# Optimization experiments

Hardware: AMD Instinct MI355X
Metric: run time of the kernel (lower is better)

## Reference

```python
import jax, jax.numpy as jnp
import numpy as np

T, B, IN, H1, H2, H3 = 128, 256, 512, 1024, 1024, 512


def _glorot(key, shape, fan):
    bound = 1.0 / np.sqrt(fan)
    return jax.random.uniform(key, shape, jnp.float32, -bound, bound)


def _cell_params(key, in_dim, h_dim):
    k = jax.random.split(key, 4)
    return (_glorot(k[0], (4 * h_dim, in_dim), h_dim),
            _glorot(k[1], (4 * h_dim, h_dim), h_dim),
            _glorot(k[2], (4 * h_dim,), h_dim),
            _glorot(k[3], (4 * h_dim,), h_dim))


def setup_inputs() -> dict:
    key = jax.random.key(0)
    ks = jax.random.split(key, 4)
    x = jax.random.normal(ks[0], (T, B, IN), jnp.float32)
    Wih1, Whh1, bih1, bhh1 = _cell_params(ks[1], IN, H1)
    Wih2, Whh2, bih2, bhh2 = _cell_params(ks[2], H1, H2)
    Wih3, Whh3, bih3, bhh3 = _cell_params(ks[3], H2, H3)
    return dict(input_seq=x,
                Wih1=Wih1, Whh1=Whh1, bih1=bih1, bhh1=bhh1,
                Wih2=Wih2, Whh2=Whh2, bih2=bih2, bhh2=bhh2,
                Wih3=Wih3, Whh3=Whh3, bih3=bih3, bhh3=bhh3)


def _lstm_cell(x, h, c, Wih, Whh, bih, bhh):
    # PyTorch LSTMCell gate order: i, f, g, o
    gates = x @ Wih.T + bih + h @ Whh.T + bhh
    i, f, g, o = jnp.split(gates, 4, axis=-1)
    c_new = jax.nn.sigmoid(f) * c + jax.nn.sigmoid(i) * jnp.tanh(g)
    h_new = jax.nn.sigmoid(o) * jnp.tanh(c_new)
    return h_new, c_new


def reference(input_seq, Wih1, Whh1, bih1, bhh1,
              Wih2, Whh2, bih2, bhh2,
              Wih3, Whh3, bih3, bhh3):
    Bn = input_seq.shape[1]
    init = (jnp.zeros((Bn, H1)), jnp.zeros((Bn, H1)),
            jnp.zeros((Bn, H2)), jnp.zeros((Bn, H2)),
            jnp.zeros((Bn, H3)), jnp.zeros((Bn, H3)))

    def step(carry, x_t):
        h1, c1, h2, c2, h3, c3 = carry
        h1, c1 = _lstm_cell(x_t, h1, c1, Wih1, Whh1, bih1, bhh1)
        h2, c2 = _lstm_cell(h1, h2, c2, Wih2, Whh2, bih2, bhh2)
        h3, c3 = _lstm_cell(h2, h3, c3, Wih3, Whh3, bih3, bhh3)
        return (h1, c1, h2, c2, h3, c3), None

    final, _ = jax.lax.scan(step, init, input_seq)
    return final
```

## Files before the change

### kernel.cpp

```cpp
#include <hip/hip_runtime.h>
#include <hip/hip_bf16.h>
#include <cstdint>
#include <cstddef>


typedef __attribute__((ext_vector_type(8))) short short8;
typedef __attribute__((ext_vector_type(4))) short short4v;
typedef __attribute__((ext_vector_type(4))) float floatx4;

#define NBLK 256
#define NTHR 1024

__device__ __forceinline__ float fsig(float x) {
    x = fminf(fmaxf(x, -30.f), 30.f);
    return 1.f / (1.f + __expf(-x));
}
__device__ __forceinline__ float ftanh(float x) {
    x = fminf(fmaxf(x, -15.f), 15.f);
    float e = __expf(2.f * x);
    return (e - 1.f) / (e + 1.f);
}

__device__ __forceinline__ int get_xcc() {
    int x;
    asm volatile("s_getreg_b32 %0, hwreg(HW_REG_XCC_ID)" : "=s"(x));
    return x & 7;
}


__device__ __forceinline__ void safe_sync(int* sy) {
    __syncthreads();
    if (threadIdx.x == 0) {
        int a = __hip_atomic_fetch_add(sy + 704, 1, __ATOMIC_ACQ_REL, __HIP_MEMORY_SCOPE_AGENT);
        if (a == NBLK - 1)
            __hip_atomic_store(sy + 768, 1, __ATOMIC_RELEASE, __HIP_MEMORY_SCOPE_AGENT);
        while (__hip_atomic_load(sy + 768, __ATOMIC_RELAXED, __HIP_MEMORY_SCOPE_AGENT) == 0)
            __builtin_amdgcn_s_sleep(2);
        __builtin_amdgcn_fence(__ATOMIC_ACQUIRE, "agent");
    }
    __syncthreads();
}

__device__ __forceinline__ void grid_sync(int* sy, int myx, int myM, int G) {
    __syncthreads();
    if (threadIdx.x == 0) {
        int* gen = sy + 576;
        int g = __hip_atomic_load(gen, __ATOMIC_RELAXED, __HIP_MEMORY_SCOPE_AGENT);
        int a = __hip_atomic_fetch_add(sy + myx * 64, 1, __ATOMIC_RELAXED, __HIP_MEMORY_SCOPE_AGENT);
        if ((a + 1) % myM == 0) {
            __builtin_amdgcn_fence(__ATOMIC_RELEASE, "agent");
            int m = __hip_atomic_fetch_add(sy + 512, 1, __ATOMIC_RELAXED, __HIP_MEMORY_SCOPE_AGENT);
            if ((m + 1) % G == 0)
                __hip_atomic_fetch_add(gen, 1, __ATOMIC_RELEASE, __HIP_MEMORY_SCOPE_AGENT);
        }
        while (__hip_atomic_load(gen, __ATOMIC_RELAXED, __HIP_MEMORY_SCOPE_AGENT) == g)
            __builtin_amdgcn_s_sleep(2);
        __builtin_amdgcn_fence(__ATOMIC_ACQUIRE, "agent");
    }
    __syncthreads();
}

template<int K1, int K2, int H>
__global__ void pack_frag_kernel(const float* __restrict__ Wih,
                                 const float* __restrict__ Whh,
                                 __hip_bfloat16* __restrict__ dst) {
    constexpr int NK = (K1 + K2) / 32;
    constexpr int NTT = H / 4;
    int idx = blockIdx.x * 256 + threadIdx.x;
    if (idx >= NTT * NK * 64) return;
    int slot = idx & 63;
    int kc = (idx >> 6) % NK;
    int b = idx / (64 * NK);
    int du = slot & 3, g = (slot >> 2) & 3, ksub = slot >> 4;
    int unit = b * 4 + du;
    int j = g * H + unit;
    int k0 = kc * 32 + ksub * 8;
    __hip_bfloat16 tmp[8];
#pragma unroll
    for (int e = 0; e < 8; ++e) {
        int k = k0 + e;
        float v = (k < K1) ? Wih[(size_t)j * K1 + k] : Whh[(size_t)j * K2 + (k - K1)];
        tmp[e] = __float2bfloat16(v);
    }
    *(short8*)(dst + (size_t)idx * 8) = *(short8*)tmp;
}

__global__ void pack_bias_kernel(const float* __restrict__ a,
                                 const float* __restrict__ b,
                                 int n, float* __restrict__ out) {
    int i = blockIdx.x * 256 + threadIdx.x;
    if (i < n) out[i] = a[i] + b[i];
}

__global__ void x_to_slab_kernel(const float* __restrict__ x,
                                 __hip_bfloat16* __restrict__ xs) {
    int idx = blockIdx.x * 256 + threadIdx.x;
    int j   = idx & 7;
    int row = (idx >> 3) & 255;
    int s   = (idx >> 11) & 63;
    int t   = idx >> 17;
    xs[idx] = __float2bfloat16(x[((size_t)(t * 256 + row)) * 512 + s * 8 + j]);
}

__global__ void zero_f32_kernel(float* p, int n) {
    int i = blockIdx.x * 256 + threadIdx.x;
    if (i < n) p[i] = 0.f;
}

__global__ void zero_i32_kernel(int* p, int n) {
    int i = blockIdx.x * 256 + threadIdx.x;
    if (i < n) p[i] = 0;
}

__device__ __forceinline__ short8 afrag8(const __hip_bfloat16* __restrict__ base, int k) {
    return *(const short8*)(base + (size_t)k * 8192);
}
__device__ __forceinline__ short8 afrag4(const __hip_bfloat16* __restrict__ base, int k) {
    const __hip_bfloat16* p = base + (size_t)k * 8192;
    short4v lo = *(const short4v*)p;
    short4v hi = *(const short4v*)(p + 1024);
    return (short8){lo.x, lo.y, lo.z, lo.w, hi.x, hi.y, hi.z, hi.w};
}

template<int NK1, int NK2, bool A2W4, int NT, int H, int TSTR>
__device__ __forceinline__ void run_layer(
    const short8* __restrict__ ldsw, int bslot0,
    const __hip_bfloat16* __restrict__ A1, const __hip_bfloat16* __restrict__ A2,
    const float (&bl)[NT],
    __hip_bfloat16* __restrict__ hs, int slab,
    float (&creg)[NT][4], int tbase, int lane, int wave,
    bool fin, float* __restrict__ ho, float* __restrict__ co)
{
    constexpr int NK = NK1 + NK2;
    constexpr int W = NT * 4;
    const int col = lane & 15, ksub = lane >> 4;
    const int row = wave * 16 + col;
    const __hip_bfloat16* __restrict__ a1 = A1 + ksub * 2048 + row * 8;
    const __hip_bfloat16* __restrict__ a2 = A2 + ksub * 2048 + (A2W4 ? row * 4 : row * 8);

    short8 rb[4];
#pragma unroll
    for (int i = 0; i < 4; ++i) rb[i] = afrag8(a1, i);

    floatx4 acc[NT];
#pragma unroll
    for (int ti = 0; ti < NT; ++ti) acc[ti] = (floatx4){0.f, 0.f, 0.f, 0.f};

#pragma unroll 4
    for (int kc = 0; kc < NK; ++kc) {
#pragma unroll
        for (int ti = 0; ti < NT; ++ti)
            acc[ti] = __builtin_amdgcn_mfma_f32_16x16x32_bf16(
                rb[kc & 3], ldsw[bslot0 + ti * TSTR + kc * 64], acc[ti], 0, 0, 0);
        int kn = kc + 4;
        if (kn < NK)
            rb[kc & 3] = (kn < NK1) ? afrag8(a1, kn)
                        : (A2W4 ? afrag4(a2, kn - NK1) : afrag8(a2, kn - NK1));
    }

    const int du = col & 3;
    const int sbase = ksub * 16 + du;
#pragma unroll
    for (int ti = 0; ti < NT; ++ti) {
        float avb[4];
#pragma unroll
        for (int r = 0; r < 4; ++r) avb[r] = acc[ti][r] + bl[ti];
#pragma unroll
        for (int r = 0; r < 4; ++r) {
            float gI = __shfl(avb[r], sbase);
            float gF = __shfl(avb[r], sbase + 4);
            float gG = __shfl(avb[r], sbase + 8);
            float gO = __shfl(avb[r], sbase + 12);
            float i_ = fsig(gI), f_ = fsig(gF), gg = ftanh(gG), o_ = fsig(gO);
            float cn = f_ * creg[ti][r] + i_ * gg;
            creg[ti][r] = cn;
            float hn = o_ * ftanh(cn);
            if (col < 4) {
                int orow = wave * 16 + ksub * 4 + r;
                hs[((size_t)slab * 256 + orow) * W + ti * 4 + du] = __float2bfloat16(hn);
                if (fin) {
                    int unit = (tbase + ti) * 4 + du;
                    ho[(size_t)orow * H + unit] = hn;
                    co[(size_t)orow * H + unit] = cn;
                }
            }
        }
    }
}

__global__ __launch_bounds__(NTHR, 4) void lstm_persistent(
    const __hip_bfloat16* __restrict__ xs,
    const __hip_bfloat16* __restrict__ w1f,
    const __hip_bfloat16* __restrict__ w2f,
    const __hip_bfloat16* __restrict__ w3f,
    const float* __restrict__ bc1, const float* __restrict__ bc2, const float* __restrict__ bc3,
    __hip_bfloat16* __restrict__ h1b, __hip_bfloat16* __restrict__ h2b,
    __hip_bfloat16* __restrict__ h3b,
    float* __restrict__ out, int* syncp)
{
    __shared__ short8 ldsw[9216];
    const int tid = threadIdx.x, blk = blockIdx.x;
    const int lane = tid & 63, wave = tid >> 6;
    const bool isA = blk < 128;
    const int sb = isA ? blk : (blk - 128);

    if (isA) {
        const short8* s2 = (const short8*)w2f + (size_t)sb * 8192;
        for (int i = tid; i < 8192; i += NTHR) ldsw[i] = s2[i];
    } else {
        const short8* s1 = (const short8*)w1f + (size_t)sb * 6144;
        for (int i = tid; i < 6144; i += NTHR) ldsw[i] = s1[i];
        const short8* s3 = (const short8*)w3f + (size_t)sb * 3072;
        for (int i = tid; i < 3072; i += NTHR) ldsw[6144 + i] = s3[i];
    }

    int myx = 0, myM = 1, G = 1;
    if (tid == 0) {
        myx = get_xcc();
        __hip_atomic_fetch_add(syncp + 640 + myx, 1, __ATOMIC_RELAXED, __HIP_MEMORY_SCOPE_AGENT);
    }
    safe_sync(syncp);
    if (tid == 0) {
        myM = __hip_atomic_load(syncp + 640 + myx, __ATOMIC_RELAXED, __HIP_MEMORY_SCOPE_AGENT);
        G = 0;
        for (int x = 0; x < 8; ++x)
            G += (__hip_atomic_load(syncp + 640 + x, __ATOMIC_RELAXED, __HIP_MEMORY_SCOPE_AGENT) > 0);
        if (myM < 1) myM = 1;
        if (G < 1) G = 1;
    }
    __syncthreads();

    const int col = lane & 15, ksub = lane >> 4, du = col & 3, g = col >> 2;
    (void)ksub; (void)col;

    float bl1[2], bl2[2], bl3[1];
    if (isA) {
        bl2[0] = bc2[g * 1024 + (2 * sb + 0) * 4 + du];
        bl2[1] = bc2[g * 1024 + (2 * sb + 1) * 4 + du];
        bl1[0] = bl1[1] = bl3[0] = 0.f;
    } else {
        bl1[0] = bc1[g * 1024 + (2 * sb + 0) * 4 + du];
        bl1[1] = bc1[g * 1024 + (2 * sb + 1) * 4 + du];
        bl3[0] = bc3[g * 512 + sb * 4 + du];
        bl2[0] = bl2[1] = 0.f;
    }

    float c1r[2][4] = {{0.f,0.f,0.f,0.f},{0.f,0.f,0.f,0.f}};
    float c2r[2][4] = {{0.f,0.f,0.f,0.f},{0.f,0.f,0.f,0.f}};
    float c3r[1][4] = {{0.f,0.f,0.f,0.f}};

    float* h1o = out;
    float* c1o = out + 262144;
    float* h2o = out + 524288;
    float* c2o = out + 786432;
    float* h3o = out + 1048576;
    float* c3o = out + 1179648;

    if (!isA) {
        run_layer<16, 32, false, 2, 1024, 3072>(ldsw, lane,
            xs, h1b + 262144, bl1, h1b, sb, c1r, 2 * sb, lane, wave, false, h1o, c1o);
    }
    grid_sync(syncp, myx, myM, G);

    for (int t = 0; t < 128; ++t) {
        const size_t cur = (size_t)(t & 1), prv = (size_t)((t + 1) & 1);
        if (isA) {
            run_layer<32, 32, false, 2, 1024, 4096>(ldsw, lane,
                h1b + cur * 262144, h2b + prv * 262144, bl2,
                h2b + cur * 262144, sb, c2r, 2 * sb, lane, wave, t == 127, h2o, c2o);
        } else {
            if (t < 127) {
                run_layer<16, 32, false, 2, 1024, 3072>(ldsw, lane,
                    xs + (size_t)(t + 1) * 131072, h1b + cur * 262144, bl1,
                    h1b + prv * 262144, sb, c1r, 2 * sb, lane, wave, (t + 1) == 127, h1o, c1o);
            }
            if (t >= 1) {
                run_layer<32, 16, true, 1, 512, 0>(ldsw, 6144 + lane,
                    h2b + prv * 262144, h3b + cur * 131072, bl3,
                    h3b + prv * 131072, sb, c3r, sb, lane, wave, false, h3o, c3o);
            }
        }
        grid_sync(syncp, myx, myM, G);
    }

    if (!isA) {
        run_layer<32, 16, true, 1, 512, 0>(ldsw, 6144 + lane,
            h2b + 262144, h3b, bl3, h3b + 131072, sb, c3r, sb, lane, wave, true, h3o, c3o);
    }
}

extern "C" void kernel_launch(void* const* d_in, const int* in_sizes, int n_in,
                              void* d_out, int out_size, void* d_ws, size_t ws_size,
                              hipStream_t stream) {
    const float* x    = (const float*)d_in[0];
    const float* Wih1 = (const float*)d_in[1];
    const float* Whh1 = (const float*)d_in[2];
    const float* bih1 = (const float*)d_in[3];
    const float* bhh1 = (const float*)d_in[4];
    const float* Wih2 = (const float*)d_in[5];
    const float* Whh2 = (const float*)d_in[6];
    const float* bih2 = (const float*)d_in[7];
    const float* bhh2 = (const float*)d_in[8];
    const float* Wih3 = (const float*)d_in[9];
    const float* Whh3 = (const float*)d_in[10];
    const float* bih3 = (const float*)d_in[11];
    const float* bhh3 = (const float*)d_in[12];
    float* out = (float*)d_out;

    char* p = (char*)d_ws;
    auto alloc = [&](size_t bytes) {
        char* r = p;
        p += (bytes + 255) & ~(size_t)255;
        return r;
    };
    __hip_bfloat16* xs  = (__hip_bfloat16*)alloc((size_t)128 * 64 * 256 * 8 * 2);
    __hip_bfloat16* w1f = (__hip_bfloat16*)alloc((size_t)256 * 48 * 64 * 8 * 2);
    __hip_bfloat16* w2f = (__hip_bfloat16*)alloc((size_t)256 * 64 * 64 * 8 * 2);
    __hip_bfloat16* w3f = (__hip_bfloat16*)alloc((size_t)128 * 48 * 64 * 8 * 2);
    float* bc1 = (float*)alloc(4096 * 4);
    float* bc2 = (float*)alloc(4096 * 4);
    float* bc3 = (float*)alloc(2048 * 4);
    __hip_bfloat16* h1b = (__hip_bfloat16*)alloc((size_t)2 * 262144 * 2);
    __hip_bfloat16* h2b = (__hip_bfloat16*)alloc((size_t)2 * 262144 * 2);
    __hip_bfloat16* h3b = (__hip_bfloat16*)alloc((size_t)2 * 131072 * 2);
    int* syncp = (int*)alloc(4096);

    auto blocks = [](int n) { return (n + 255) / 256; };

    pack_frag_kernel<512, 1024, 1024><<<blocks(256 * 48 * 64), 256, 0, stream>>>(Wih1, Whh1, w1f);
    pack_frag_kernel<1024, 1024, 1024><<<blocks(256 * 64 * 64), 256, 0, stream>>>(Wih2, Whh2, w2f);
    pack_frag_kernel<1024, 512, 512><<<blocks(128 * 48 * 64), 256, 0, stream>>>(Wih3, Whh3, w3f);
    pack_bias_kernel<<<blocks(4096), 256, 0, stream>>>(bih1, bhh1, 4096, bc1);
    pack_bias_kernel<<<blocks(4096), 256, 0, stream>>>(bih2, bhh2, 4096, bc2);
    pack_bias_kernel<<<blocks(2048), 256, 0, stream>>>(bih3, bhh3, 2048, bc3);
    x_to_slab_kernel<<<blocks(128 * 256 * 512), 256, 0, stream>>>(x, xs);
    zero_f32_kernel<<<blocks(262144), 256, 0, stream>>>((float*)h1b, 262144);
    zero_f32_kernel<<<blocks(262144), 256, 0, stream>>>((float*)h2b, 262144);
    zero_f32_kernel<<<blocks(131072), 256, 0, stream>>>((float*)h3b, 131072);
    zero_i32_kernel<<<1, 1024, 0, stream>>>(syncp, 1024);

    lstm_persistent<<<NBLK, NTHR, 0, stream>>>(xs, w1f, w2f, w3f, bc1, bc2, bc3,
                                               h1b, h2b, h3b, out, syncp);
}
```

Baseline: 3.981 ms.

## Stage hidden states into per-XCC scratch copies with XCC-local barrier

Each timestep, the blocks on an XCC now cooperatively copy the shared h1/h2/h3 bf16 state buffers into a private per-XCC scratch region, using device-scope atomic loads. They then synchronise through an XCC-local counter plus buffer_inv before running the layers from that copy. The intent is that repeated reads of hidden state hit the local L2 instead of crossing XCCs. Hidden-state stores become packed 32-bit atomic stores, and the grid barrier's release/acquire fences are removed. The change adds an extra copy and barrier per step, and dropping the fences risks memory-ordering bugs.

```diff
diff --git a/kernel.cpp b/kernel.cpp
--- a/kernel.cpp
+++ b/kernel.cpp
@@ -10,6 +10,8 @@
 
 #define NBLK 256
 #define NTHR 1024
+
+#define SCR_BYTES 1310720
 
 __device__ __forceinline__ float fsig(float x) {
     x = fminf(fmaxf(x, -30.f), 30.f);
@@ -48,16 +50,36 @@
         int g = __hip_atomic_load(gen, __ATOMIC_RELAXED, __HIP_MEMORY_SCOPE_AGENT);
         int a = __hip_atomic_fetch_add(sy + myx * 64, 1, __ATOMIC_RELAXED, __HIP_MEMORY_SCOPE_AGENT);
         if ((a + 1) % myM == 0) {
-            __builtin_amdgcn_fence(__ATOMIC_RELEASE, "agent");
             int m = __hip_atomic_fetch_add(sy + 512, 1, __ATOMIC_RELAXED, __HIP_MEMORY_SCOPE_AGENT);
             if ((m + 1) % G == 0)
-                __hip_atomic_fetch_add(gen, 1, __ATOMIC_RELEASE, __HIP_MEMORY_SCOPE_AGENT);
+                __hip_atomic_fetch_add(gen, 1, __ATOMIC_RELAXED, __HIP_MEMORY_SCOPE_AGENT);
         }
         while (__hip_atomic_load(gen, __ATOMIC_RELAXED, __HIP_MEMORY_SCOPE_AGENT) == g)
             __builtin_amdgcn_s_sleep(2);
-        __builtin_amdgcn_fence(__ATOMIC_ACQUIRE, "agent");
-    }
-    __syncthreads();
+    }
+    __syncthreads();
+}
+
+__device__ __forceinline__ void stage_sync(int* sy, int myx, int myM, int round) {
+    __syncthreads();
+    if (threadIdx.x == 0) {
+        int* c = sy + 832 + myx * 16;
+        __hip_atomic_fetch_add(c, 1, __ATOMIC_RELAXED, __HIP_MEMORY_SCOPE_AGENT);
+        int tgt = myM * round;
+        while (__hip_atomic_load(c, __ATOMIC_RELAXED, __HIP_MEMORY_SCOPE_AGENT) < tgt)
+            __builtin_amdgcn_s_sleep(1);
+        asm volatile("buffer_inv sc0\n\ts_waitcnt vmcnt(0)" ::: "memory");
+    }
+    __syncthreads();
+}
+
+__device__ __forceinline__ void stage_buf8(const unsigned long long* __restrict__ src,
+                                           unsigned long long* __restrict__ dst,
+                                           int n8, int r, int m) {
+    int lo = (int)((long long)n8 * r / m);
+    int hi = (int)((long long)n8 * (r + 1) / m);
+    for (int i = lo + (int)threadIdx.x; i < hi; i += NTHR)
+        dst[i] = __hip_atomic_load(src + i, __ATOMIC_RELAXED, __HIP_MEMORY_SCOPE_AGENT);
 }
 
 template<int K1, int K2, int H>
@@ -175,9 +197,17 @@
             float cn = f_ * creg[ti][r] + i_ * gg;
             creg[ti][r] = cn;
             float hn = o_ * ftanh(cn);
+            __hip_bfloat16 hv = __float2bfloat16(hn);
+            unsigned hb = (unsigned)*reinterpret_cast<unsigned short*>(&hv);
+            unsigned hp = __shfl(hb, lane + 1);
+            int orow = wave * 16 + ksub * 4 + r;
             if (col < 4) {
-                int orow = wave * 16 + ksub * 4 + r;
-                hs[((size_t)slab * 256 + orow) * W + ti * 4 + du] = __float2bfloat16(hn);
+                if ((col & 1) == 0) {
+                    unsigned pk = hb | (hp << 16);
+                    size_t idx = ((size_t)slab * 256 + orow) * W + ti * 4 + col;
+                    __hip_atomic_store((unsigned*)(hs + idx), pk,
+                                       __ATOMIC_RELAXED, __HIP_MEMORY_SCOPE_AGENT);
+                }
                 if (fin) {
                     int unit = (tbase + ti) * 4 + du;
                     ho[(size_t)orow * H + unit] = hn;
@@ -196,9 +226,11 @@
     const float* __restrict__ bc1, const float* __restrict__ bc2, const float* __restrict__ bc3,
     __hip_bfloat16* __restrict__ h1b, __hip_bfloat16* __restrict__ h2b,
     __hip_bfloat16* __restrict__ h3b,
+    __hip_bfloat16* __restrict__ scr,
     float* __restrict__ out, int* syncp)
 {
     __shared__ short8 ldsw[9216];
+    __shared__ int smeta[4];
     const int tid = threadIdx.x, blk = blockIdx.x;
     const int lane = tid & 63, wave = tid >> 6;
     const bool isA = blk < 128;
@@ -217,7 +249,9 @@
     int myx = 0, myM = 1, G = 1;
     if (tid == 0) {
         myx = get_xcc();
-        __hip_atomic_fetch_add(syncp + 640 + myx, 1, __ATOMIC_RELAXED, __HIP_MEMORY_SCOPE_AGENT);
+        int r = __hip_atomic_fetch_add(syncp + 640 + myx, 1, __ATOMIC_RELAXED, __HIP_MEMORY_SCOPE_AGENT);
+        smeta[0] = myx;
+        smeta[2] = r;
     }
     safe_sync(syncp);
     if (tid == 0) {
@@ -227,8 +261,16 @@
             G += (__hip_atomic_load(syncp + 640 + x, __ATOMIC_RELAXED, __HIP_MEMORY_SCOPE_AGENT) > 0);
         if (myM < 1) myM = 1;
         if (G < 1) G = 1;
-    }
-    __syncthreads();
+        smeta[1] = myM;
+    }
+    __syncthreads();
+    const int myx_a = smeta[0];
+    const int myM_a = smeta[1];
+    const int myr_a = smeta[2];
+
+    __hip_bfloat16* sc1 = scr + (size_t)myx_a * (SCR_BYTES / 2);
+    __hip_bfloat16* sc2 = sc1 + 262144;
+    __hip_bfloat16* sc3 = sc2 + 262144;
 
     const int col = lane & 15, ksub = lane >> 4, du = col & 3, g = col >> 2;
     (void)ksub; (void)col;
@@ -260,32 +302,46 @@
         run_layer<16, 32, false, 2, 1024, 3072>(ldsw, lane,
             xs, h1b + 262144, bl1, h1b, sb, c1r, 2 * sb, lane, wave, false, h1o, c1o);
     }
-    grid_sync(syncp, myx, myM, G);
+    grid_sync(syncp, myx_a, myM_a, G);
 
     for (int t = 0; t < 128; ++t) {
         const size_t cur = (size_t)(t & 1), prv = (size_t)((t + 1) & 1);
+
+        stage_buf8((const unsigned long long*)(h1b + cur * 262144),
+                   (unsigned long long*)sc1, 65536, myr_a, myM_a);
+        stage_buf8((const unsigned long long*)(h2b + prv * 262144),
+                   (unsigned long long*)sc2, 65536, myr_a, myM_a);
+        stage_buf8((const unsigned long long*)(h3b + cur * 131072),
+                   (unsigned long long*)sc3, 32768, myr_a, myM_a);
+        stage_sync(syncp, myx_a, myM_a, t + 1);
+
         if (isA) {
             run_layer<32, 32, false, 2, 1024, 4096>(ldsw, lane,
-                h1b + cur * 262144, h2b + prv * 262144, bl2,
+                sc1, sc2, bl2,
                 h2b + cur * 262144, sb, c2r, 2 * sb, lane, wave, t == 127, h2o, c2o);
         } else {
             if (t < 127) {
                 run_layer<16, 32, false, 2, 1024, 3072>(ldsw, lane,
-                    xs + (size_t)(t + 1) * 131072, h1b + cur * 262144, bl1,
+                    xs + (size_t)(t + 1) * 131072, sc1, bl1,
                     h1b + prv * 262144, sb, c1r, 2 * sb, lane, wave, (t + 1) == 127, h1o, c1o);
             }
             if (t >= 1) {
                 run_layer<32, 16, true, 1, 512, 0>(ldsw, 6144 + lane,
-                    h2b + prv * 262144, h3b + cur * 131072, bl3,
+                    sc2, sc3, bl3,
                     h3b + prv * 131072, sb, c3r, sb, lane, wave, false, h3o, c3o);
             }
         }
-        grid_sync(syncp, myx, myM, G);
-    }
-
+        grid_sync(syncp, myx_a, myM_a, G);
+    }
+
+    stage_buf8((const unsigned long long*)(h2b + 262144),
+               (unsigned long long*)sc2, 65536, myr_a, myM_a);
+    stage_buf8((const unsigned long long*)h3b,
+               (unsigned long long*)sc3, 32768, myr_a, myM_a);
+    stage_sync(syncp, myx_a, myM_a, 129);
     if (!isA) {
         run_layer<32, 16, true, 1, 512, 0>(ldsw, 6144 + lane,
-            h2b + 262144, h3b, bl3, h3b + 131072, sb, c3r, sb, lane, wave, true, h3o, c3o);
+            sc2, sc3, bl3, h3b + 131072, sb, c3r, sb, lane, wave, true, h3o, c3o);
     }
 }
 
@@ -323,6 +379,7 @@
     __hip_bfloat16* h1b = (__hip_bfloat16*)alloc((size_t)2 * 262144 * 2);
     __hip_bfloat16* h2b = (__hip_bfloat16*)alloc((size_t)2 * 262144 * 2);
     __hip_bfloat16* h3b = (__hip_bfloat16*)alloc((size_t)2 * 131072 * 2);
+    __hip_bfloat16* scr = (__hip_bfloat16*)alloc((size_t)8 * SCR_BYTES);
     int* syncp = (int*)alloc(4096);
 
     auto blocks = [](int n) { return (n + 255) / 256; };
@@ -340,5 +397,5 @@
     zero_i32_kernel<<<1, 1024, 0, stream>>>(syncp, 1024);
 
     lstm_persistent<<<NBLK, NTHR, 0, stream>>>(xs, w1f, w2f, w3f, bc1, bc2, bc3,
-                                               h1b, h2b, h3b, out, syncp);
-}
+                                               h1b, h2b, h3b, scr, out, syncp);
+}
```

After: 4.419 ms. +11.0%, slower.

## Elect one block per XCC to acquire, others wait on per-XCC epoch

Applied to the files above, without the earlier changes.

Rewrites the grid barrier so only the first block on each XCC does the agent-scope acquire fence and then publishes a per-XCC epoch. The other blocks spin on that epoch and run a local buffer_inv. The release fences are dropped, and hidden-state bf16 writes become packed 32-bit relaxed atomic stores made with a lane shuffle. The aim is to cut cache-invalidate and fence cost at each of the 129 grid barriers. In exchange, memory-ordering correctness now relies on relaxed atomics plus manual cache invalidation, and there is an extra serial hop per XCC.

```diff
diff --git a/kernel.cpp b/kernel.cpp
--- a/kernel.cpp
+++ b/kernel.cpp
@@ -41,21 +41,29 @@
     __syncthreads();
 }
 
-__device__ __forceinline__ void grid_sync(int* sy, int myx, int myM, int G) {
+__device__ __forceinline__ void grid_sync(int* sy, int myx, int myM, int G,
+                                          int myr, int round) {
     __syncthreads();
     if (threadIdx.x == 0) {
         int* gen = sy + 576;
         int g = __hip_atomic_load(gen, __ATOMIC_RELAXED, __HIP_MEMORY_SCOPE_AGENT);
         int a = __hip_atomic_fetch_add(sy + myx * 64, 1, __ATOMIC_RELAXED, __HIP_MEMORY_SCOPE_AGENT);
         if ((a + 1) % myM == 0) {
-            __builtin_amdgcn_fence(__ATOMIC_RELEASE, "agent");
             int m = __hip_atomic_fetch_add(sy + 512, 1, __ATOMIC_RELAXED, __HIP_MEMORY_SCOPE_AGENT);
             if ((m + 1) % G == 0)
-                __hip_atomic_fetch_add(gen, 1, __ATOMIC_RELEASE, __HIP_MEMORY_SCOPE_AGENT);
+                __hip_atomic_fetch_add(gen, 1, __ATOMIC_RELAXED, __HIP_MEMORY_SCOPE_AGENT);
         }
         while (__hip_atomic_load(gen, __ATOMIC_RELAXED, __HIP_MEMORY_SCOPE_AGENT) == g)
             __builtin_amdgcn_s_sleep(2);
-        __builtin_amdgcn_fence(__ATOMIC_ACQUIRE, "agent");
+        int* ep = sy + 832 + myx * 16;
+        if (myr == 0) {
+            __builtin_amdgcn_fence(__ATOMIC_ACQUIRE, "agent");
+            __hip_atomic_store(ep, round, __ATOMIC_RELEASE, __HIP_MEMORY_SCOPE_AGENT);
+        } else {
+            while (__hip_atomic_load(ep, __ATOMIC_RELAXED, __HIP_MEMORY_SCOPE_AGENT) < round)
+                __builtin_amdgcn_s_sleep(1);
+            asm volatile("buffer_inv sc0\n\ts_waitcnt vmcnt(0)" ::: "memory");
+        }
     }
     __syncthreads();
 }
@@ -175,9 +183,17 @@
             float cn = f_ * creg[ti][r] + i_ * gg;
             creg[ti][r] = cn;
             float hn = o_ * ftanh(cn);
+            __hip_bfloat16 hv = __float2bfloat16(hn);
+            unsigned hb = (unsigned)*reinterpret_cast<unsigned short*>(&hv);
+            unsigned hp = __shfl(hb, lane + 1);
+            int orow = wave * 16 + ksub * 4 + r;
             if (col < 4) {
-                int orow = wave * 16 + ksub * 4 + r;
-                hs[((size_t)slab * 256 + orow) * W + ti * 4 + du] = __float2bfloat16(hn);
+                if ((col & 1) == 0) {
+                    unsigned pk = hb | (hp << 16);
+                    size_t idx = ((size_t)slab * 256 + orow) * W + ti * 4 + col;
+                    __hip_atomic_store((unsigned*)(hs + idx), pk,
+                                       __ATOMIC_RELAXED, __HIP_MEMORY_SCOPE_AGENT);
+                }
                 if (fin) {
                     int unit = (tbase + ti) * 4 + du;
                     ho[(size_t)orow * H + unit] = hn;
@@ -199,6 +215,7 @@
     float* __restrict__ out, int* syncp)
 {
     __shared__ short8 ldsw[9216];
+    __shared__ int smeta[4];
     const int tid = threadIdx.x, blk = blockIdx.x;
     const int lane = tid & 63, wave = tid >> 6;
     const bool isA = blk < 128;
@@ -217,7 +234,9 @@
     int myx = 0, myM = 1, G = 1;
     if (tid == 0) {
         myx = get_xcc();
-        __hip_atomic_fetch_add(syncp + 640 + myx, 1, __ATOMIC_RELAXED, __HIP_MEMORY_SCOPE_AGENT);
+        int r = __hip_atomic_fetch_add(syncp + 640 + myx, 1, __ATOMIC_RELAXED, __HIP_MEMORY_SCOPE_AGENT);
+        smeta[0] = myx;
+        smeta[2] = r;
     }
     safe_sync(syncp);
     if (tid == 0) {
@@ -227,8 +246,12 @@
             G += (__hip_atomic_load(syncp + 640 + x, __ATOMIC_RELAXED, __HIP_MEMORY_SCOPE_AGENT) > 0);
         if (myM < 1) myM = 1;
         if (G < 1) G = 1;
-    }
-    __syncthreads();
+        smeta[1] = myM;
+    }
+    __syncthreads();
+    const int myx_a = smeta[0];
+    const int myM_a = smeta[1];
+    const int myr_a = smeta[2];
 
     const int col = lane & 15, ksub = lane >> 4, du = col & 3, g = col >> 2;
     (void)ksub; (void)col;
@@ -260,7 +283,7 @@
         run_layer<16, 32, false, 2, 1024, 3072>(ldsw, lane,
             xs, h1b + 262144, bl1, h1b, sb, c1r, 2 * sb, lane, wave, false, h1o, c1o);
     }
-    grid_sync(syncp, myx, myM, G);
+    grid_sync(syncp, myx_a, myM_a, G, myr_a, 1);
 
     for (int t = 0; t < 128; ++t) {
         const size_t cur = (size_t)(t & 1), prv = (size_t)((t + 1) & 1);
@@ -280,7 +303,7 @@
                     h3b + prv * 131072, sb, c3r, sb, lane, wave, false, h3o, c3o);
             }
         }
-        grid_sync(syncp, myx, myM, G);
+        grid_sync(syncp, myx_a, myM_a, G, myr_a, t + 2);
     }
 
     if (!isA) {
```

After: 3.833 ms. 1.04x faster.

## Replace persistent grid-synced kernel with per-step launches and global cell state

Applied to the files above, without the earlier changes.

Drops the persistent kernel and its atomic grid barrier. It launches one kernel per wavefront phase (130 launches), with cell state kept in global memory between launches and weights restaged into LDS on each launch through global_load_lds. It also deepens the A-fragment prefetch from 4 to 8 and packs pairs of bf16 h outputs into 32-bit stores. The intent is to replace the custom spin barrier with kernel boundaries, at the cost of launch overhead, reloading weights every step, and extra c-state traffic.

```diff
diff --git a/kernel.cpp b/kernel.cpp
--- a/kernel.cpp
+++ b/kernel.cpp
@@ -8,7 +8,6 @@
 typedef __attribute__((ext_vector_type(4))) short short4v;
 typedef __attribute__((ext_vector_type(4))) float floatx4;
 
-#define NBLK 256
 #define NTHR 1024
 
 __device__ __forceinline__ float fsig(float x) {
@@ -21,43 +20,11 @@
     return (e - 1.f) / (e + 1.f);
 }
 
-__device__ __forceinline__ int get_xcc() {
-    int x;
-    asm volatile("s_getreg_b32 %0, hwreg(HW_REG_XCC_ID)" : "=s"(x));
-    return x & 7;
-}
-
-
-__device__ __forceinline__ void safe_sync(int* sy) {
-    __syncthreads();
-    if (threadIdx.x == 0) {
-        int a = __hip_atomic_fetch_add(sy + 704, 1, __ATOMIC_ACQ_REL, __HIP_MEMORY_SCOPE_AGENT);
-        if (a == NBLK - 1)
-            __hip_atomic_store(sy + 768, 1, __ATOMIC_RELEASE, __HIP_MEMORY_SCOPE_AGENT);
-        while (__hip_atomic_load(sy + 768, __ATOMIC_RELAXED, __HIP_MEMORY_SCOPE_AGENT) == 0)
-            __builtin_amdgcn_s_sleep(2);
-        __builtin_amdgcn_fence(__ATOMIC_ACQUIRE, "agent");
-    }
-    __syncthreads();
-}
-
-__device__ __forceinline__ void grid_sync(int* sy, int myx, int myM, int G) {
-    __syncthreads();
-    if (threadIdx.x == 0) {
-        int* gen = sy + 576;
-        int g = __hip_atomic_load(gen, __ATOMIC_RELAXED, __HIP_MEMORY_SCOPE_AGENT);
-        int a = __hip_atomic_fetch_add(sy + myx * 64, 1, __ATOMIC_RELAXED, __HIP_MEMORY_SCOPE_AGENT);
-        if ((a + 1) % myM == 0) {
-            __builtin_amdgcn_fence(__ATOMIC_RELEASE, "agent");
-            int m = __hip_atomic_fetch_add(sy + 512, 1, __ATOMIC_RELAXED, __HIP_MEMORY_SCOPE_AGENT);
-            if ((m + 1) % G == 0)
-                __hip_atomic_fetch_add(gen, 1, __ATOMIC_RELEASE, __HIP_MEMORY_SCOPE_AGENT);
-        }
-        while (__hip_atomic_load(gen, __ATOMIC_RELAXED, __HIP_MEMORY_SCOPE_AGENT) == g)
-            __builtin_amdgcn_s_sleep(2);
-        __builtin_amdgcn_fence(__ATOMIC_ACQUIRE, "agent");
-    }
-    __syncthreads();
+__device__ __forceinline__ void stage16(const void* gptr, void* lptr) {
+    __builtin_amdgcn_global_load_lds(
+        (const __attribute__((address_space(1))) unsigned int*)gptr,
+        (__attribute__((address_space(3))) unsigned int*)lptr,
+        16, 0, 0);
 }
 
 template<int K1, int K2, int H>
@@ -107,11 +74,6 @@
     if (i < n) p[i] = 0.f;
 }
 
-__global__ void zero_i32_kernel(int* p, int n) {
-    int i = blockIdx.x * 256 + threadIdx.x;
-    if (i < n) p[i] = 0;
-}
-
 __device__ __forceinline__ short8 afrag8(const __hip_bfloat16* __restrict__ base, int k) {
     return *(const short8*)(base + (size_t)k * 8192);
 }
@@ -138,23 +100,23 @@
     const __hip_bfloat16* __restrict__ a1 = A1 + ksub * 2048 + row * 8;
     const __hip_bfloat16* __restrict__ a2 = A2 + ksub * 2048 + (A2W4 ? row * 4 : row * 8);
 
-    short8 rb[4];
-#pragma unroll
-    for (int i = 0; i < 4; ++i) rb[i] = afrag8(a1, i);
+    short8 rb[8];
+#pragma unroll
+    for (int i = 0; i < 8; ++i) rb[i] = afrag8(a1, i);
 
     floatx4 acc[NT];
 #pragma unroll
     for (int ti = 0; ti < NT; ++ti) acc[ti] = (floatx4){0.f, 0.f, 0.f, 0.f};
 
-#pragma unroll 4
+#pragma unroll 8
     for (int kc = 0; kc < NK; ++kc) {
 #pragma unroll
         for (int ti = 0; ti < NT; ++ti)
             acc[ti] = __builtin_amdgcn_mfma_f32_16x16x32_bf16(
-                rb[kc & 3], ldsw[bslot0 + ti * TSTR + kc * 64], acc[ti], 0, 0, 0);
-        int kn = kc + 4;
+                rb[kc & 7], ldsw[bslot0 + ti * TSTR + kc * 64], acc[ti], 0, 0, 0);
+        int kn = kc + 8;
         if (kn < NK)
-            rb[kc & 3] = (kn < NK1) ? afrag8(a1, kn)
+            rb[kc & 7] = (kn < NK1) ? afrag8(a1, kn)
                         : (A2W4 ? afrag4(a2, kn - NK1) : afrag8(a2, kn - NK1));
     }
 
@@ -175,9 +137,16 @@
             float cn = f_ * creg[ti][r] + i_ * gg;
             creg[ti][r] = cn;
             float hn = o_ * ftanh(cn);
+            __hip_bfloat16 hv = __float2bfloat16(hn);
+            unsigned hb = (unsigned)*reinterpret_cast<unsigned short*>(&hv);
+            unsigned hp = __shfl(hb, lane + 1);
+            int orow = wave * 16 + ksub * 4 + r;
             if (col < 4) {
-                int orow = wave * 16 + ksub * 4 + r;
-                hs[((size_t)slab * 256 + orow) * W + ti * 4 + du] = __float2bfloat16(hn);
+                if ((col & 1) == 0) {
+                    unsigned pk = hb | (hp << 16);
+                    size_t idx = ((size_t)slab * 256 + orow) * W + ti * 4 + col;
+                    *(unsigned*)(hs + idx) = pk;
+                }
                 if (fin) {
                     int unit = (tbase + ti) * 4 + du;
                     ho[(size_t)orow * H + unit] = hn;
@@ -188,7 +157,7 @@
     }
 }
 
-__global__ __launch_bounds__(NTHR, 4) void lstm_persistent(
+__global__ __launch_bounds__(NTHR, 4) void lstm_step(
     const __hip_bfloat16* __restrict__ xs,
     const __hip_bfloat16* __restrict__ w1f,
     const __hip_bfloat16* __restrict__ w2f,
@@ -196,7 +165,8 @@
     const float* __restrict__ bc1, const float* __restrict__ bc2, const float* __restrict__ bc3,
     __hip_bfloat16* __restrict__ h1b, __hip_bfloat16* __restrict__ h2b,
     __hip_bfloat16* __restrict__ h3b,
-    float* __restrict__ out, int* syncp)
+    float* __restrict__ c1s, float* __restrict__ c2s, float* __restrict__ c3s,
+    float* __restrict__ out, int p)
 {
     __shared__ short8 ldsw[9216];
     const int tid = threadIdx.x, blk = blockIdx.x;
@@ -204,50 +174,61 @@
     const bool isA = blk < 128;
     const int sb = isA ? blk : (blk - 128);
 
+    if (isA && (p < 0 || p > 127)) return;
+
     if (isA) {
-        const short8* s2 = (const short8*)w2f + (size_t)sb * 8192;
-        for (int i = tid; i < 8192; i += NTHR) ldsw[i] = s2[i];
+        const char* gw = (const char*)w2f + (size_t)sb * 131072;
+#pragma unroll
+        for (int c = 0; c < 8; ++c)
+            stage16(gw + ((size_t)((wave * 8 + c) * 64 + lane) * 16),
+                    (char*)ldsw + (size_t)(wave * 8 + c) * 1024);
     } else {
-        const short8* s1 = (const short8*)w1f + (size_t)sb * 6144;
-        for (int i = tid; i < 6144; i += NTHR) ldsw[i] = s1[i];
-        const short8* s3 = (const short8*)w3f + (size_t)sb * 3072;
-        for (int i = tid; i < 3072; i += NTHR) ldsw[6144 + i] = s3[i];
-    }
-
-    int myx = 0, myM = 1, G = 1;
-    if (tid == 0) {
-        myx = get_xcc();
-        __hip_atomic_fetch_add(syncp + 640 + myx, 1, __ATOMIC_RELAXED, __HIP_MEMORY_SCOPE_AGENT);
-    }
-    safe_sync(syncp);
-    if (tid == 0) {
-        myM = __hip_atomic_load(syncp + 640 + myx, __ATOMIC_RELAXED, __HIP_MEMORY_SCOPE_AGENT);
-        G = 0;
-        for (int x = 0; x < 8; ++x)
-            G += (__hip_atomic_load(syncp + 640 + x, __ATOMIC_RELAXED, __HIP_MEMORY_SCOPE_AGENT) > 0);
-        if (myM < 1) myM = 1;
-        if (G < 1) G = 1;
-    }
-    __syncthreads();
+        if (p <= 126) {
+            const char* g1 = (const char*)w1f + (size_t)sb * 98304;
+#pragma unroll
+            for (int c = 0; c < 6; ++c)
+                stage16(g1 + ((size_t)((wave * 6 + c) * 64 + lane) * 16),
+                        (char*)ldsw + (size_t)(wave * 6 + c) * 1024);
+        }
+        if (p >= 1) {
+            const char* g3 = (const char*)w3f + (size_t)sb * 49152;
+#pragma unroll
+            for (int c = 0; c < 3; ++c)
+                stage16(g3 + ((size_t)((wave * 3 + c) * 64 + lane) * 16),
+                        (char*)ldsw + 98304 + (size_t)(wave * 3 + c) * 1024);
+        }
+    }
 
     const int col = lane & 15, ksub = lane >> 4, du = col & 3, g = col >> 2;
-    (void)ksub; (void)col;
+    const int orow0 = wave * 16 + ksub * 4;
 
     float bl1[2], bl2[2], bl3[1];
+    float c1r[2][4], c2r[2][4], c3r[1][4];
+
     if (isA) {
         bl2[0] = bc2[g * 1024 + (2 * sb + 0) * 4 + du];
         bl2[1] = bc2[g * 1024 + (2 * sb + 1) * 4 + du];
-        bl1[0] = bl1[1] = bl3[0] = 0.f;
+#pragma unroll
+        for (int ti = 0; ti < 2; ++ti)
+#pragma unroll
+            for (int r = 0; r < 4; ++r)
+                c2r[ti][r] = c2s[((size_t)sb * 256 + orow0 + r) * 8 + ti * 4 + du];
     } else {
         bl1[0] = bc1[g * 1024 + (2 * sb + 0) * 4 + du];
         bl1[1] = bc1[g * 1024 + (2 * sb + 1) * 4 + du];
         bl3[0] = bc3[g * 512 + sb * 4 + du];
-        bl2[0] = bl2[1] = 0.f;
-    }
-
-    float c1r[2][4] = {{0.f,0.f,0.f,0.f},{0.f,0.f,0.f,0.f}};
-    float c2r[2][4] = {{0.f,0.f,0.f,0.f},{0.f,0.f,0.f,0.f}};
-    float c3r[1][4] = {{0.f,0.f,0.f,0.f}};
+#pragma unroll
+        for (int ti = 0; ti < 2; ++ti)
+#pragma unroll
+            for (int r = 0; r < 4; ++r)
+                c1r[ti][r] = c1s[((size_t)sb * 256 + orow0 + r) * 8 + ti * 4 + du];
+#pragma unroll
+        for (int r = 0; r < 4; ++r)
+            c3r[0][r] = c3s[((size_t)sb * 256 + orow0 + r) * 4 + du];
+    }
+
+    asm volatile("s_waitcnt vmcnt(0)" ::: "memory");
+    __syncthreads();
 
     float* h1o = out;
     float* c1o = out + 262144;
@@ -256,36 +237,42 @@
     float* h3o = out + 1048576;
     float* c3o = out + 1179648;
 
-    if (!isA) {
-        run_layer<16, 32, false, 2, 1024, 3072>(ldsw, lane,
-            xs, h1b + 262144, bl1, h1b, sb, c1r, 2 * sb, lane, wave, false, h1o, c1o);
-    }
-    grid_sync(syncp, myx, myM, G);
-
-    for (int t = 0; t < 128; ++t) {
-        const size_t cur = (size_t)(t & 1), prv = (size_t)((t + 1) & 1);
-        if (isA) {
-            run_layer<32, 32, false, 2, 1024, 4096>(ldsw, lane,
-                h1b + cur * 262144, h2b + prv * 262144, bl2,
-                h2b + cur * 262144, sb, c2r, 2 * sb, lane, wave, t == 127, h2o, c2o);
-        } else {
-            if (t < 127) {
-                run_layer<16, 32, false, 2, 1024, 3072>(ldsw, lane,
-                    xs + (size_t)(t + 1) * 131072, h1b + cur * 262144, bl1,
-                    h1b + prv * 262144, sb, c1r, 2 * sb, lane, wave, (t + 1) == 127, h1o, c1o);
+    const size_t cur = (size_t)(p & 1), prv = (size_t)((p + 1) & 1);
+
+    if (isA) {
+        run_layer<32, 32, false, 2, 1024, 4096>(ldsw, lane,
+            h1b + cur * 262144, h2b + prv * 262144, bl2,
+            h2b + cur * 262144, sb, c2r, 2 * sb, lane, wave, p == 127, h2o, c2o);
+        if (col < 4) {
+#pragma unroll
+            for (int ti = 0; ti < 2; ++ti)
+#pragma unroll
+                for (int r = 0; r < 4; ++r)
+                    c2s[((size_t)sb * 256 + orow0 + r) * 8 + ti * 4 + du] = c2r[ti][r];
+        }
+    } else {
+        if (p <= 126) {
+            run_layer<16, 32, false, 2, 1024, 3072>(ldsw, lane,
+                xs + (size_t)(p + 1) * 131072, h1b + cur * 262144, bl1,
+                h1b + prv * 262144, sb, c1r, 2 * sb, lane, wave, (p + 1) == 127, h1o, c1o);
+            if (col < 4) {
+#pragma unroll
+                for (int ti = 0; ti < 2; ++ti)
+#pragma unroll
+                    for (int r = 0; r < 4; ++r)
+                        c1s[((size_t)sb * 256 + orow0 + r) * 8 + ti * 4 + du] = c1r[ti][r];
             }
-            if (t >= 1) {
-                run_layer<32, 16, true, 1, 512, 0>(ldsw, 6144 + lane,
-                    h2b + prv * 262144, h3b + cur * 131072, bl3,
-                    h3b + prv * 131072, sb, c3r, sb, lane, wave, false, h3o, c3o);
+        }
+        if (p >= 1) {
+            run_layer<32, 16, true, 1, 512, 0>(ldsw, 6144 + lane,
+                h2b + prv * 262144, h3b + cur * 131072, bl3,
+                h3b + prv * 131072, sb, c3r, sb, lane, wave, p == 128, h3o, c3o);
+            if (col < 4) {
+#pragma unroll
+                for (int r = 0; r < 4; ++r)
+                    c3s[((size_t)sb * 256 + orow0 + r) * 4 + du] = c3r[0][r];
             }
         }
-        grid_sync(syncp, myx, myM, G);
-    }
-
-    if (!isA) {
-        run_layer<32, 16, true, 1, 512, 0>(ldsw, 6144 + lane,
-            h2b + 262144, h3b, bl3, h3b + 131072, sb, c3r, sb, lane, wave, true, h3o, c3o);
     }
 }
 
@@ -323,7 +310,9 @@
     __hip_bfloat16* h1b = (__hip_bfloat16*)alloc((size_t)2 * 262144 * 2);
     __hip_bfloat16* h2b = (__hip_bfloat16*)alloc((size_t)2 * 262144 * 2);
     __hip_bfloat16* h3b = (__hip_bfloat16*)alloc((size_t)2 * 131072 * 2);
-    int* syncp = (int*)alloc(4096);
+    float* c1s = (float*)alloc((size_t)262144 * 4);
+    float* c2s = (float*)alloc((size_t)262144 * 4);
+    float* c3s = (float*)alloc((size_t)131072 * 4);
 
     auto blocks = [](int n) { return (n + 255) / 256; };
 
@@ -337,8 +326,11 @@
     zero_f32_kernel<<<blocks(262144), 256, 0, stream>>>((float*)h1b, 262144);
     zero_f32_kernel<<<blocks(262144), 256, 0, stream>>>((float*)h2b, 262144);
     zero_f32_kernel<<<blocks(131072), 256, 0, stream>>>((float*)h3b, 131072);
-    zero_i32_kernel<<<1, 1024, 0, stream>>>(syncp, 1024);
-
-    lstm_persistent<<<NBLK, NTHR, 0, stream>>>(xs, w1f, w2f, w3f, bc1, bc2, bc3,
-                                               h1b, h2b, h3b, out, syncp);
-}
+    zero_f32_kernel<<<blocks(262144), 256, 0, stream>>>(c1s, 262144);
+    zero_f32_kernel<<<blocks(262144), 256, 0, stream>>>(c2s, 262144);
+    zero_f32_kernel<<<blocks(131072), 256, 0, stream>>>(c3s, 131072);
+
+    for (int ph = -1; ph <= 128; ++ph)
+        lstm_step<<<256, NTHR, 0, stream>>>(xs, w1f, w2f, w3f, bc1, bc2, bc3,
+                                            h1b, h2b, h3b, c1s, c2s, c3s, out, ph);
+}
```

Result: no change. 4.025 ms (+1.1%).
